# Kernel tuning notes

Hardware: AMD Instinct MI355X
Metric: run time of the kernel (lower is better)

The kernel has to match this reference:

```python
import jax, jax.numpy as jnp
import numpy as np

NEG_SLOPE = 0.2
EPS = 1e-16


def gat_conv(x, src, dst, W, a_src, a_dst, b, num_nodes):
    # Single-head PyG GATConv (heads=1, add_self_loops already applied via src/dst).
    h = x @ W                                   # [N, C]
    alpha_s = h @ a_src                         # [N]
    alpha_d = h @ a_dst                         # [N]
    e = jax.nn.leaky_relu(alpha_s[src] + alpha_d[dst], NEG_SLOPE)  # [E]
    # softmax over incoming edges per destination node
    m = jax.ops.segment_max(e, dst, num_segments=num_nodes)        # [N]
    ex = jnp.exp(e - m[dst])
    denom = jax.ops.segment_sum(ex, dst, num_segments=num_nodes)   # [N]
    alpha = ex / (denom[dst] + EPS)                                 # [E]
    out = jax.ops.segment_sum(h[src] * alpha[:, None], dst, num_segments=num_nodes)
    return out + b


def setup_inputs() -> dict:
    key = jax.random.key(0)
    ks = jax.random.split(key, 10)
    N, E, F_in, H, C = 100000, 1600000, 64, 64, 32
    x = jax.random.normal(ks[0], (N, F_in), dtype=jnp.float32)
    edge_index = jax.random.randint(ks[1], (2, E), 0, N, dtype=jnp.int64)
    s1 = 1.0 / np.sqrt(F_in)
    s2 = 1.0 / np.sqrt(H)
    return {
        "x": x,
        "edge_index": edge_index,
        "W1": jax.random.normal(ks[2], (F_in, H), dtype=jnp.float32) * s1,
        "a1_src": jax.random.normal(ks[3], (H,), dtype=jnp.float32) * s2,
        "a1_dst": jax.random.normal(ks[4], (H,), dtype=jnp.float32) * s2,
        "b1": jnp.zeros((H,), dtype=jnp.float32),
        "W2": jax.random.normal(ks[5], (H, C), dtype=jnp.float32) * s2,
        "a2_src": jax.random.normal(ks[6], (C,), dtype=jnp.float32) / np.sqrt(C),
        "a2_dst": jax.random.normal(ks[7], (C,), dtype=jnp.float32) / np.sqrt(C),
        "b2": jnp.zeros((C,), dtype=jnp.float32),
    }


def reference(x, edge_index, W1, a1_src, a1_dst, b1, W2, a2_src, a2_dst, b2):
    N = x.shape[0]
    loops = jnp.arange(N, dtype=edge_index.dtype)
    src = jnp.concatenate([edge_index[0], loops])  # add self-loops (GATConv default)
    dst = jnp.concatenate([edge_index[1], loops])
    # dropout layers are no-ops in eval mode
    h = jax.nn.relu(gat_conv(x, src, dst, W1, a1_src, a1_dst, b1, N))
    out = gat_conv(h, src, dst, W2, a2_src, a2_dst, b2, N)
    return jax.nn.log_softmax(out, axis=-1)
```

## Files before the change

kernel.cpp:

```cpp
#include <hip/hip_runtime.h>

typedef unsigned int uint;
typedef unsigned short ushort;
typedef short short8 __attribute__((ext_vector_type(8)));
typedef float floatx4 __attribute__((ext_vector_type(4)));

#define LEAKY(e) ((e) > 0.f ? (e) : 0.2f * (e))
#define BCAP 6144
#define EPT 32
#define TILE (256 * EPT)

__device__ __forceinline__ ushort f2bf(float f) {
    uint u = __float_as_uint(f);
    return (ushort)((u + 0x7fffu + ((u >> 16) & 1u)) >> 16);
}
__device__ __forceinline__ float bflo(uint u) { return __uint_as_float(u << 16); }
__device__ __forceinline__ float bfhi(uint u) { return __uint_as_float(u & 0xffff0000u); }

__global__ __launch_bounds__(256) void gemm1_mfma(
    const float* __restrict__ x, const float* __restrict__ W,
    const float* __restrict__ a_src, const float* __restrict__ a_dst,
    ushort* __restrict__ hb, float* __restrict__ as, float* __restrict__ ad, int N)
{
    int tid = threadIdx.x;
    int wave = tid >> 6, lane = tid & 63;
    int q = lane >> 4, c0 = lane & 15;
    int rowbase = blockIdx.x * 64 + wave * 16;
    int arow = rowbase + c0;
    bool aok = arow < N;

    short8 afrag[2];
#pragma unroll
    for (int kb = 0; kb < 2; ++kb) {
        float xa[8];
        if (aok) {
            const float4 u0 = *(const float4*)(x + (size_t)arow * 64 + kb * 32 + q * 8);
            const float4 u1 = *(const float4*)(x + (size_t)arow * 64 + kb * 32 + q * 8 + 4);
            xa[0] = u0.x; xa[1] = u0.y; xa[2] = u0.z; xa[3] = u0.w;
            xa[4] = u1.x; xa[5] = u1.y; xa[6] = u1.z; xa[7] = u1.w;
        } else {
#pragma unroll
            for (int j = 0; j < 8; ++j) xa[j] = 0.f;
        }
#pragma unroll
        for (int j = 0; j < 8; ++j) afrag[kb][j] = (short)f2bf(xa[j]);
    }

    short8 bfrag[4][2];
#pragma unroll
    for (int t = 0; t < 4; ++t)
#pragma unroll
        for (int kb = 0; kb < 2; ++kb)
#pragma unroll
            for (int j = 0; j < 8; ++j)
                bfrag[t][kb][j] = (short)f2bf(W[(size_t)(kb * 32 + q * 8 + j) * 64 + t * 16 + c0]);

    floatx4 acc[4];
#pragma unroll
    for (int t = 0; t < 4; ++t) acc[t] = (floatx4){0.f, 0.f, 0.f, 0.f};
#pragma unroll
    for (int t = 0; t < 4; ++t)
#pragma unroll
        for (int kb = 0; kb < 2; ++kb)
            acc[t] = __builtin_amdgcn_mfma_f32_16x16x32_bf16(afrag[kb], bfrag[t][kb], acc[t], 0, 0, 0);

    float a_s[4], a_d[4];
#pragma unroll
    for (int t = 0; t < 4; ++t) { a_s[t] = a_src[t * 16 + c0]; a_d[t] = a_dst[t * 16 + c0]; }
    float vs[4], vd[4];
#pragma unroll
    for (int r = 0; r < 4; ++r) {
        vs[r] = 0.f; vd[r] = 0.f;
#pragma unroll
        for (int t = 0; t < 4; ++t) { vs[r] += acc[t][r] * a_s[t]; vd[r] += acc[t][r] * a_d[t]; }
    }
#pragma unroll
    for (int o = 1; o < 16; o <<= 1)
#pragma unroll
        for (int r = 0; r < 4; ++r) {
            vs[r] += __shfl_xor(vs[r], o, 16);
            vd[r] += __shfl_xor(vd[r], o, 16);
        }
    int drow = rowbase + q * 4;
    if (c0 == 0) {
#pragma unroll
        for (int r = 0; r < 4; ++r)
            if (drow + r < N) { as[drow + r] = vs[r]; ad[drow + r] = vd[r]; }
    }
#pragma unroll
    for (int r = 0; r < 4; ++r) {
        if (drow + r < N) {
#pragma unroll
            for (int t = 0; t < 4; ++t)
                hb[(size_t)(drow + r) * 64 + t * 16 + c0] = f2bf(acc[t][r]);
        }
    }
}

__global__ __launch_bounds__(256) void gemm2_mfma(
    const float* __restrict__ agg1, const float* __restrict__ b1,
    const float* __restrict__ W,
    const float* __restrict__ a_src, const float* __restrict__ a_dst,
    ushort* __restrict__ hb, float* __restrict__ as, float* __restrict__ ad, int N)
{
    int tid = threadIdx.x;
    int wave = tid >> 6, lane = tid & 63;
    int q = lane >> 4, c0 = lane & 15;
    int rowbase = blockIdx.x * 64 + wave * 16;
    int arow = rowbase + c0;
    bool aok = arow < N;

    short8 afrag[2];
#pragma unroll
    for (int kb = 0; kb < 2; ++kb) {
        float xa[8];
        const float4 b0 = *(const float4*)(b1 + kb * 32 + q * 8);
        const float4 b4 = *(const float4*)(b1 + kb * 32 + q * 8 + 4);
        if (aok) {
            const float4 u0 = *(const float4*)(agg1 + (size_t)arow * 64 + kb * 32 + q * 8);
            const float4 u1 = *(const float4*)(agg1 + (size_t)arow * 64 + kb * 32 + q * 8 + 4);
            xa[0] = u0.x + b0.x; xa[1] = u0.y + b0.y; xa[2] = u0.z + b0.z; xa[3] = u0.w + b0.w;
            xa[4] = u1.x + b4.x; xa[5] = u1.y + b4.y; xa[6] = u1.z + b4.z; xa[7] = u1.w + b4.w;
#pragma unroll
            for (int j = 0; j < 8; ++j) xa[j] = xa[j] > 0.f ? xa[j] : 0.f;
        } else {
#pragma unroll
            for (int j = 0; j < 8; ++j) xa[j] = 0.f;
        }
#pragma unroll
        for (int j = 0; j < 8; ++j) afrag[kb][j] = (short)f2bf(xa[j]);
    }

    short8 bfrag[2][2];
#pragma unroll
    for (int t = 0; t < 2; ++t)
#pragma unroll
        for (int kb = 0; kb < 2; ++kb)
#pragma unroll
            for (int j = 0; j < 8; ++j)
                bfrag[t][kb][j] = (short)f2bf(W[(size_t)(kb * 32 + q * 8 + j) * 32 + t * 16 + c0]);

    floatx4 acc[2];
#pragma unroll
    for (int t = 0; t < 2; ++t) acc[t] = (floatx4){0.f, 0.f, 0.f, 0.f};
#pragma unroll
    for (int t = 0; t < 2; ++t)
#pragma unroll
        for (int kb = 0; kb < 2; ++kb)
            acc[t] = __builtin_amdgcn_mfma_f32_16x16x32_bf16(afrag[kb], bfrag[t][kb], acc[t], 0, 0, 0);

    float a_s[2], a_d[2];
#pragma unroll
    for (int t = 0; t < 2; ++t) { a_s[t] = a_src[t * 16 + c0]; a_d[t] = a_dst[t * 16 + c0]; }
    float vs[4], vd[4];
#pragma unroll
    for (int r = 0; r < 4; ++r) {
        vs[r] = 0.f; vd[r] = 0.f;
#pragma unroll
        for (int t = 0; t < 2; ++t) { vs[r] += acc[t][r] * a_s[t]; vd[r] += acc[t][r] * a_d[t]; }
    }
#pragma unroll
    for (int o = 1; o < 16; o <<= 1)
#pragma unroll
        for (int r = 0; r < 4; ++r) {
            vs[r] += __shfl_xor(vs[r], o, 16);
            vd[r] += __shfl_xor(vd[r], o, 16);
        }
    int drow = rowbase + q * 4;
    if (c0 == 0) {
#pragma unroll
        for (int r = 0; r < 4; ++r)
            if (drow + r < N) { as[drow + r] = vs[r]; ad[drow + r] = vd[r]; }
    }
#pragma unroll
    for (int r = 0; r < 4; ++r) {
        if (drow + r < N) {
#pragma unroll
            for (int t = 0; t < 2; ++t)
                hb[(size_t)(drow + r) * 32 + t * 16 + c0] = f2bf(acc[t][r]);
        }
    }
}

__global__ __launch_bounds__(256) void binK(
    const int* __restrict__ srcA, const int* __restrict__ dstA,
    int* __restrict__ bcur, int* __restrict__ binned, int E, int Etot, int nbuck)
{
    __shared__ int hist[512];
    __shared__ int basep[512];
    int t = threadIdx.x;
    long long start = (long long)blockIdx.x * TILE;

    hist[t] = 0; hist[t + 256] = 0;
    __syncthreads();

    short bs[EPT];
    int vals[EPT];
#pragma unroll
    for (int j = 0; j < EPT; ++j) {
        long long i = start + (long long)j * 256 + t;
        if (i < Etot) {
            int s, d;
            if (i < E) { s = srcA[i]; d = dstA[i]; } else { s = d = (int)(i - E); }
            int b = d >> 8;
            bs[j] = (short)b;
            vals[j] = (s << 8) | (d & 255);
            atomicAdd(&hist[b], 1);
        } else bs[j] = -1;
    }
    __syncthreads();

    for (int b = t; b < nbuck; b += 256) {
        int hc = hist[b];
        basep[b] = hc ? atomicAdd(bcur + b * 16, hc) : 0;
    }
    __syncthreads();
    hist[t] = 0; hist[t + 256] = 0;
    __syncthreads();

#pragma unroll
    for (int j = 0; j < EPT; ++j) {
        int b = bs[j];
        if (b >= 0) {
            int pos = basep[b] + atomicAdd(&hist[b], 1);
            if (pos < BCAP) binned[(size_t)b * BCAP + pos] = vals[j];
        }
    }
}

__global__ __launch_bounds__(256) void bucketK(
    const int* __restrict__ bcur, const int* __restrict__ binned,
    int* __restrict__ off, int* __restrict__ csr, int N, int nbuck)
{
    __shared__ int hist[256];
    __shared__ int sh[256];
    __shared__ int cur[256];
    int b = blockIdx.x;
    int t = threadIdx.x;
    int cnt = min(bcur[b * 16], BCAP);
    const int* bin = binned + (size_t)b * BCAP;

    int partial = 0;
    for (int i = t; i < b; i += 256) partial += min(bcur[i * 16], BCAP);
    sh[t] = partial;
    __syncthreads();
#pragma unroll
    for (int o = 128; o > 0; o >>= 1) {
        if (t < o) sh[t] += sh[t + o];
        __syncthreads();
    }
    int base = sh[0];
    __syncthreads();

    hist[t] = 0;
    __syncthreads();
    for (int i = t; i < cnt; i += 256) atomicAdd(&hist[bin[i] & 255], 1);
    __syncthreads();
    int v = hist[t];
    sh[t] = v;
    __syncthreads();
#pragma unroll
    for (int o = 1; o < 256; o <<= 1) {
        int u = (t >= o) ? sh[t - o] : 0;
        __syncthreads();
        sh[t] += u;
        __syncthreads();
    }
    int excl = sh[t] - v;
    int d = b * 256 + t;
    if (d < N) off[d] = base + excl;
    if (b == nbuck - 1 && t == 0) off[N] = base + cnt;
    cur[t] = base + excl;
    __syncthreads();
    for (int i = t; i < cnt; i += 256) {
        int e = bin[i];
        int p = atomicAdd(&cur[e & 255], 1);
        csr[p] = e >> 8;
    }
}

__global__ __launch_bounds__(256) void node_agg1(
    const int* __restrict__ csr_src, const int* __restrict__ off,
    const float* __restrict__ as, const float* __restrict__ ad,
    const ushort* __restrict__ hb, float* __restrict__ agg, int N)
{
    int tid = threadIdx.x;
    int lid = tid & 7;
    int n = blockIdx.x * 32 + (tid >> 3);
    if (n >= N) return;
    int p0 = off[n], p1 = off[n + 1];
    float adn = ad[n];

    float den = 0.f;
    float acc[8];
#pragma unroll
    for (int k = 0; k < 8; ++k) acc[k] = 0.f;

    int p = p0;
    for (; p + 3 < p1; p += 4) {
        int s0 = csr_src[p], s1 = csr_src[p + 1], s2 = csr_src[p + 2], s3 = csr_src[p + 3];
        float e0 = as[s0], e1 = as[s1], e2 = as[s2], e3 = as[s3];
        const uint4 v0 = *(const uint4*)(hb + (size_t)s0 * 64 + lid * 8);
        const uint4 v1 = *(const uint4*)(hb + (size_t)s1 * 64 + lid * 8);
        const uint4 v2 = *(const uint4*)(hb + (size_t)s2 * 64 + lid * 8);
        const uint4 v3 = *(const uint4*)(hb + (size_t)s3 * 64 + lid * 8);
        float w0 = __expf(LEAKY(e0 + adn));
        float w1 = __expf(LEAKY(e1 + adn));
        float w2 = __expf(LEAKY(e2 + adn));
        float w3 = __expf(LEAKY(e3 + adn));
        den += (w0 + w1) + (w2 + w3);
        acc[0] += w0 * bflo(v0.x); acc[1] += w0 * bfhi(v0.x);
        acc[2] += w0 * bflo(v0.y); acc[3] += w0 * bfhi(v0.y);
        acc[4] += w0 * bflo(v0.z); acc[5] += w0 * bfhi(v0.z);
        acc[6] += w0 * bflo(v0.w); acc[7] += w0 * bfhi(v0.w);
        acc[0] += w1 * bflo(v1.x); acc[1] += w1 * bfhi(v1.x);
        acc[2] += w1 * bflo(v1.y); acc[3] += w1 * bfhi(v1.y);
        acc[4] += w1 * bflo(v1.z); acc[5] += w1 * bfhi(v1.z);
        acc[6] += w1 * bflo(v1.w); acc[7] += w1 * bfhi(v1.w);
        acc[0] += w2 * bflo(v2.x); acc[1] += w2 * bfhi(v2.x);
        acc[2] += w2 * bflo(v2.y); acc[3] += w2 * bfhi(v2.y);
        acc[4] += w2 * bflo(v2.z); acc[5] += w2 * bfhi(v2.z);
        acc[6] += w2 * bflo(v2.w); acc[7] += w2 * bfhi(v2.w);
        acc[0] += w3 * bflo(v3.x); acc[1] += w3 * bfhi(v3.x);
        acc[2] += w3 * bflo(v3.y); acc[3] += w3 * bfhi(v3.y);
        acc[4] += w3 * bflo(v3.z); acc[5] += w3 * bfhi(v3.z);
        acc[6] += w3 * bflo(v3.w); acc[7] += w3 * bfhi(v3.w);
    }
    for (; p < p1; ++p) {
        int s0 = csr_src[p];
        float w0 = __expf(LEAKY(as[s0] + adn));
        const uint4 v0 = *(const uint4*)(hb + (size_t)s0 * 64 + lid * 8);
        den += w0;
        acc[0] += w0 * bflo(v0.x); acc[1] += w0 * bfhi(v0.x);
        acc[2] += w0 * bflo(v0.y); acc[3] += w0 * bfhi(v0.y);
        acc[4] += w0 * bflo(v0.z); acc[5] += w0 * bfhi(v0.z);
        acc[6] += w0 * bflo(v0.w); acc[7] += w0 * bfhi(v0.w);
    }
    float inv = 1.f / den;
    float4 o0 = make_float4(acc[0] * inv, acc[1] * inv, acc[2] * inv, acc[3] * inv);
    float4 o1 = make_float4(acc[4] * inv, acc[5] * inv, acc[6] * inv, acc[7] * inv);
    float* op = agg + (size_t)n * 64 + lid * 8;
    *(float4*)op = o0;
    *(float4*)(op + 4) = o1;
}

__global__ __launch_bounds__(256) void node_agg2(
    const int* __restrict__ csr_src, const int* __restrict__ off,
    const float* __restrict__ as, const float* __restrict__ ad,
    const ushort* __restrict__ hb, const float* __restrict__ b2,
    float* __restrict__ out, int N)
{
    int tid = threadIdx.x;
    int lid = tid & 3;
    int n = blockIdx.x * 64 + (tid >> 2);
    if (n >= N) return;
    int p0 = off[n], p1 = off[n + 1];
    float adn = ad[n];

    float den = 0.f;
    float acc[8];
#pragma unroll
    for (int k = 0; k < 8; ++k) acc[k] = 0.f;

    int p = p0;
    for (; p + 3 < p1; p += 4) {
        int s0 = csr_src[p], s1 = csr_src[p + 1], s2 = csr_src[p + 2], s3 = csr_src[p + 3];
        float e0 = as[s0], e1 = as[s1], e2 = as[s2], e3 = as[s3];
        const uint4 v0 = *(const uint4*)(hb + (size_t)s0 * 32 + lid * 8);
        const uint4 v1 = *(const uint4*)(hb + (size_t)s1 * 32 + lid * 8);
        const uint4 v2 = *(const uint4*)(hb + (size_t)s2 * 32 + lid * 8);
        const uint4 v3 = *(const uint4*)(hb + (size_t)s3 * 32 + lid * 8);
        float w0 = __expf(LEAKY(e0 + adn));
        float w1 = __expf(LEAKY(e1 + adn));
        float w2 = __expf(LEAKY(e2 + adn));
        float w3 = __expf(LEAKY(e3 + adn));
        den += (w0 + w1) + (w2 + w3);
        acc[0] += w0 * bflo(v0.x); acc[1] += w0 * bfhi(v0.x);
        acc[2] += w0 * bflo(v0.y); acc[3] += w0 * bfhi(v0.y);
        acc[4] += w0 * bflo(v0.z); acc[5] += w0 * bfhi(v0.z);
        acc[6] += w0 * bflo(v0.w); acc[7] += w0 * bfhi(v0.w);
        acc[0] += w1 * bflo(v1.x); acc[1] += w1 * bfhi(v1.x);
        acc[2] += w1 * bflo(v1.y); acc[3] += w1 * bfhi(v1.y);
        acc[4] += w1 * bflo(v1.z); acc[5] += w1 * bfhi(v1.z);
        acc[6] += w1 * bflo(v1.w); acc[7] += w1 * bfhi(v1.w);
        acc[0] += w2 * bflo(v2.x); acc[1] += w2 * bfhi(v2.x);
        acc[2] += w2 * bflo(v2.y); acc[3] += w2 * bfhi(v2.y);
        acc[4] += w2 * bflo(v2.z); acc[5] += w2 * bfhi(v2.z);
        acc[6] += w2 * bflo(v2.w); acc[7] += w2 * bfhi(v2.w);
        acc[0] += w3 * bflo(v3.x); acc[1] += w3 * bfhi(v3.x);
        acc[2] += w3 * bflo(v3.y); acc[3] += w3 * bfhi(v3.y);
        acc[4] += w3 * bflo(v3.z); acc[5] += w3 * bfhi(v3.z);
        acc[6] += w3 * bflo(v3.w); acc[7] += w3 * bfhi(v3.w);
    }
    for (; p < p1; ++p) {
        int s0 = csr_src[p];
        float w0 = __expf(LEAKY(as[s0] + adn));
        const uint4 v0 = *(const uint4*)(hb + (size_t)s0 * 32 + lid * 8);
        den += w0;
        acc[0] += w0 * bflo(v0.x); acc[1] += w0 * bfhi(v0.x);
        acc[2] += w0 * bflo(v0.y); acc[3] += w0 * bfhi(v0.y);
        acc[4] += w0 * bflo(v0.z); acc[5] += w0 * bfhi(v0.z);
        acc[6] += w0 * bflo(v0.w); acc[7] += w0 * bfhi(v0.w);
    }
    float inv = 1.f / den;
#pragma unroll
    for (int k = 0; k < 8; ++k) acc[k] = acc[k] * inv + b2[lid * 8 + k];

    float mx = acc[0];
#pragma unroll
    for (int k = 1; k < 8; ++k) mx = fmaxf(mx, acc[k]);
#pragma unroll
    for (int o = 2; o > 0; o >>= 1) mx = fmaxf(mx, __shfl_xor(mx, o, 4));
    float se = 0.f;
#pragma unroll
    for (int k = 0; k < 8; ++k) se += __expf(acc[k] - mx);
#pragma unroll
    for (int o = 2; o > 0; o >>= 1) se += __shfl_xor(se, o, 4);
    float lse = mx + __logf(se);
    float4 o0 = make_float4(acc[0] - lse, acc[1] - lse, acc[2] - lse, acc[3] - lse);
    float4 o1 = make_float4(acc[4] - lse, acc[5] - lse, acc[6] - lse, acc[7] - lse);
    float* op = out + (size_t)n * 32 + lid * 8;
    *(float4*)op = o0;
    *(float4*)(op + 4) = o1;
}

extern "C" void kernel_launch(void* const* d_in, const int* in_sizes, int n_in,
                              void* d_out, int out_size, void* d_ws, size_t ws_size,
                              hipStream_t stream) {
    const float* x   = (const float*)d_in[0];
    const int*   ei  = (const int*)d_in[1];
    const float* W1  = (const float*)d_in[2];
    const float* a1s = (const float*)d_in[3];
    const float* a1d = (const float*)d_in[4];
    const float* b1  = (const float*)d_in[5];
    const float* W2  = (const float*)d_in[6];
    const float* a2s = (const float*)d_in[7];
    const float* a2d = (const float*)d_in[8];
    const float* b2  = (const float*)d_in[9];

    int N = in_sizes[0] / 64;
    int E = in_sizes[1] / 2;
    int Etot = E + N;
    int nbuck = (N + 255) >> 8;
    const int* srcA = ei;
    const int* dstA = ei + E;

    float* ws = (float*)d_ws;
    ushort* hb1 = (ushort*)ws;
    float* agg1 = ws + (size_t)N * 32;
    ushort* hb2 = (ushort*)(agg1 + (size_t)N * 64);
    float* as1  = agg1 + (size_t)N * 64 + (size_t)N * 16;
    float* ad1  = as1 + N;
    float* as2  = ad1 + N;
    float* ad2  = as2 + N;
    int* off    = (int*)(ad2 + N);
    int* bcur   = off + (N + 1);
    int* csr    = bcur + (size_t)nbuck * 16;
    int* binned = csr + Etot;

    hipMemsetAsync(bcur, 0, sizeof(int) * (size_t)nbuck * 16, stream);

    int tb = (int)(((long long)Etot + TILE - 1) / TILE);
    binK<<<tb, 256, 0, stream>>>(srcA, dstA, bcur, binned, E, Etot, nbuck);
    bucketK<<<nbuck, 256, 0, stream>>>(bcur, binned, off, csr, N, nbuck);

    gemm1_mfma<<<(N + 63) / 64, 256, 0, stream>>>(x, W1, a1s, a1d, hb1, as1, ad1, N);
    node_agg1<<<(N + 31) / 32, 256, 0, stream>>>(csr, off, as1, ad1, hb1, agg1, N);

    gemm2_mfma<<<(N + 63) / 64, 256, 0, stream>>>(agg1, b1, W2, a2s, a2d, hb2, as2, ad2, N);
    node_agg2<<<(N + 63) / 64, 256, 0, stream>>>(csr, off, as2, ad2, hb2, b2,
                                                 (float*)d_out, N);
}
```

Measured before the change: 225.1 us.

## Fuse edge binning with first GEMM, cooperative edge gathers, bf16 layer-1 aggregate

```diff
diff --git a/kernel.cpp b/kernel.cpp
--- a/kernel.cpp
+++ b/kernel.cpp
@@ -14,182 +14,20 @@
     uint u = __float_as_uint(f);
     return (ushort)((u + 0x7fffu + ((u >> 16) & 1u)) >> 16);
 }
+__device__ __forceinline__ uint pack2bf(float lo, float hi) {
+    return (uint)f2bf(lo) | ((uint)f2bf(hi) << 16);
+}
 __device__ __forceinline__ float bflo(uint u) { return __uint_as_float(u << 16); }
 __device__ __forceinline__ float bfhi(uint u) { return __uint_as_float(u & 0xffff0000u); }
 
-__global__ __launch_bounds__(256) void gemm1_mfma(
-    const float* __restrict__ x, const float* __restrict__ W,
-    const float* __restrict__ a_src, const float* __restrict__ a_dst,
-    ushort* __restrict__ hb, float* __restrict__ as, float* __restrict__ ad, int N)
-{
-    int tid = threadIdx.x;
-    int wave = tid >> 6, lane = tid & 63;
-    int q = lane >> 4, c0 = lane & 15;
-    int rowbase = blockIdx.x * 64 + wave * 16;
-    int arow = rowbase + c0;
-    bool aok = arow < N;
-
-    short8 afrag[2];
-#pragma unroll
-    for (int kb = 0; kb < 2; ++kb) {
-        float xa[8];
-        if (aok) {
-            const float4 u0 = *(const float4*)(x + (size_t)arow * 64 + kb * 32 + q * 8);
-            const float4 u1 = *(const float4*)(x + (size_t)arow * 64 + kb * 32 + q * 8 + 4);
-            xa[0] = u0.x; xa[1] = u0.y; xa[2] = u0.z; xa[3] = u0.w;
-            xa[4] = u1.x; xa[5] = u1.y; xa[6] = u1.z; xa[7] = u1.w;
-        } else {
-#pragma unroll
-            for (int j = 0; j < 8; ++j) xa[j] = 0.f;
-        }
-#pragma unroll
-        for (int j = 0; j < 8; ++j) afrag[kb][j] = (short)f2bf(xa[j]);
-    }
-
-    short8 bfrag[4][2];
-#pragma unroll
-    for (int t = 0; t < 4; ++t)
-#pragma unroll
-        for (int kb = 0; kb < 2; ++kb)
-#pragma unroll
-            for (int j = 0; j < 8; ++j)
-                bfrag[t][kb][j] = (short)f2bf(W[(size_t)(kb * 32 + q * 8 + j) * 64 + t * 16 + c0]);
-
-    floatx4 acc[4];
-#pragma unroll
-    for (int t = 0; t < 4; ++t) acc[t] = (floatx4){0.f, 0.f, 0.f, 0.f};
-#pragma unroll
-    for (int t = 0; t < 4; ++t)
-#pragma unroll
-        for (int kb = 0; kb < 2; ++kb)
-            acc[t] = __builtin_amdgcn_mfma_f32_16x16x32_bf16(afrag[kb], bfrag[t][kb], acc[t], 0, 0, 0);
-
-    float a_s[4], a_d[4];
-#pragma unroll
-    for (int t = 0; t < 4; ++t) { a_s[t] = a_src[t * 16 + c0]; a_d[t] = a_dst[t * 16 + c0]; }
-    float vs[4], vd[4];
-#pragma unroll
-    for (int r = 0; r < 4; ++r) {
-        vs[r] = 0.f; vd[r] = 0.f;
-#pragma unroll
-        for (int t = 0; t < 4; ++t) { vs[r] += acc[t][r] * a_s[t]; vd[r] += acc[t][r] * a_d[t]; }
-    }
-#pragma unroll
-    for (int o = 1; o < 16; o <<= 1)
-#pragma unroll
-        for (int r = 0; r < 4; ++r) {
-            vs[r] += __shfl_xor(vs[r], o, 16);
-            vd[r] += __shfl_xor(vd[r], o, 16);
-        }
-    int drow = rowbase + q * 4;
-    if (c0 == 0) {
-#pragma unroll
-        for (int r = 0; r < 4; ++r)
-            if (drow + r < N) { as[drow + r] = vs[r]; ad[drow + r] = vd[r]; }
-    }
-#pragma unroll
-    for (int r = 0; r < 4; ++r) {
-        if (drow + r < N) {
-#pragma unroll
-            for (int t = 0; t < 4; ++t)
-                hb[(size_t)(drow + r) * 64 + t * 16 + c0] = f2bf(acc[t][r]);
-        }
-    }
-}
-
-__global__ __launch_bounds__(256) void gemm2_mfma(
-    const float* __restrict__ agg1, const float* __restrict__ b1,
-    const float* __restrict__ W,
-    const float* __restrict__ a_src, const float* __restrict__ a_dst,
-    ushort* __restrict__ hb, float* __restrict__ as, float* __restrict__ ad, int N)
-{
-    int tid = threadIdx.x;
-    int wave = tid >> 6, lane = tid & 63;
-    int q = lane >> 4, c0 = lane & 15;
-    int rowbase = blockIdx.x * 64 + wave * 16;
-    int arow = rowbase + c0;
-    bool aok = arow < N;
-
-    short8 afrag[2];
-#pragma unroll
-    for (int kb = 0; kb < 2; ++kb) {
-        float xa[8];
-        const float4 b0 = *(const float4*)(b1 + kb * 32 + q * 8);
-        const float4 b4 = *(const float4*)(b1 + kb * 32 + q * 8 + 4);
-        if (aok) {
-            const float4 u0 = *(const float4*)(agg1 + (size_t)arow * 64 + kb * 32 + q * 8);
-            const float4 u1 = *(const float4*)(agg1 + (size_t)arow * 64 + kb * 32 + q * 8 + 4);
-            xa[0] = u0.x + b0.x; xa[1] = u0.y + b0.y; xa[2] = u0.z + b0.z; xa[3] = u0.w + b0.w;
-            xa[4] = u1.x + b4.x; xa[5] = u1.y + b4.y; xa[6] = u1.z + b4.z; xa[7] = u1.w + b4.w;
-#pragma unroll
-            for (int j = 0; j < 8; ++j) xa[j] = xa[j] > 0.f ? xa[j] : 0.f;
-        } else {
-#pragma unroll
-            for (int j = 0; j < 8; ++j) xa[j] = 0.f;
-        }
-#pragma unroll
-        for (int j = 0; j < 8; ++j) afrag[kb][j] = (short)f2bf(xa[j]);
-    }
-
-    short8 bfrag[2][2];
-#pragma unroll
-    for (int t = 0; t < 2; ++t)
-#pragma unroll
-        for (int kb = 0; kb < 2; ++kb)
-#pragma unroll
-            for (int j = 0; j < 8; ++j)
-                bfrag[t][kb][j] = (short)f2bf(W[(size_t)(kb * 32 + q * 8 + j) * 32 + t * 16 + c0]);
-
-    floatx4 acc[2];
-#pragma unroll
-    for (int t = 0; t < 2; ++t) acc[t] = (floatx4){0.f, 0.f, 0.f, 0.f};
-#pragma unroll
-    for (int t = 0; t < 2; ++t)
-#pragma unroll
-        for (int kb = 0; kb < 2; ++kb)
-            acc[t] = __builtin_amdgcn_mfma_f32_16x16x32_bf16(afrag[kb], bfrag[t][kb], acc[t], 0, 0, 0);
-
-    float a_s[2], a_d[2];
-#pragma unroll
-    for (int t = 0; t < 2; ++t) { a_s[t] = a_src[t * 16 + c0]; a_d[t] = a_dst[t * 16 + c0]; }
-    float vs[4], vd[4];
-#pragma unroll
-    for (int r = 0; r < 4; ++r) {
-        vs[r] = 0.f; vd[r] = 0.f;
-#pragma unroll
-        for (int t = 0; t < 2; ++t) { vs[r] += acc[t][r] * a_s[t]; vd[r] += acc[t][r] * a_d[t]; }
-    }
-#pragma unroll
-    for (int o = 1; o < 16; o <<= 1)
-#pragma unroll
-        for (int r = 0; r < 4; ++r) {
-            vs[r] += __shfl_xor(vs[r], o, 16);
-            vd[r] += __shfl_xor(vd[r], o, 16);
-        }
-    int drow = rowbase + q * 4;
-    if (c0 == 0) {
-#pragma unroll
-        for (int r = 0; r < 4; ++r)
-            if (drow + r < N) { as[drow + r] = vs[r]; ad[drow + r] = vd[r]; }
-    }
-#pragma unroll
-    for (int r = 0; r < 4; ++r) {
-        if (drow + r < N) {
-#pragma unroll
-            for (int t = 0; t < 2; ++t)
-                hb[(size_t)(drow + r) * 32 + t * 16 + c0] = f2bf(acc[t][r]);
-        }
-    }
-}
-
-__global__ __launch_bounds__(256) void binK(
-    const int* __restrict__ srcA, const int* __restrict__ dstA,
+__device__ __forceinline__ void binK_body(
+    int bid, const int* __restrict__ srcA, const int* __restrict__ dstA,
     int* __restrict__ bcur, int* __restrict__ binned, int E, int Etot, int nbuck)
 {
     __shared__ int hist[512];
     __shared__ int basep[512];
     int t = threadIdx.x;
-    long long start = (long long)blockIdx.x * TILE;
+    long long start = (long long)bid * TILE;
 
     hist[t] = 0; hist[t + 256] = 0;
     __syncthreads();
@@ -228,6 +66,184 @@
     }
 }
 
+__device__ __forceinline__ void gemm1_body(
+    int bid, const float* __restrict__ x, const float* __restrict__ W,
+    const float* __restrict__ a_src, const float* __restrict__ a_dst,
+    ushort* __restrict__ hb, float* __restrict__ as, float* __restrict__ ad, int N)
+{
+    int tid = threadIdx.x;
+    int wave = tid >> 6, lane = tid & 63;
+    int q = lane >> 4, c0 = lane & 15;
+    int rowbase = bid * 64 + wave * 16;
+    int arow = rowbase + c0;
+    bool aok = arow < N;
+
+    short8 afrag[2];
+#pragma unroll
+    for (int kb = 0; kb < 2; ++kb) {
+        float xa[8];
+        if (aok) {
+            const float4 u0 = *(const float4*)(x + (size_t)arow * 64 + kb * 32 + q * 8);
+            const float4 u1 = *(const float4*)(x + (size_t)arow * 64 + kb * 32 + q * 8 + 4);
+            xa[0] = u0.x; xa[1] = u0.y; xa[2] = u0.z; xa[3] = u0.w;
+            xa[4] = u1.x; xa[5] = u1.y; xa[6] = u1.z; xa[7] = u1.w;
+        } else {
+#pragma unroll
+            for (int j = 0; j < 8; ++j) xa[j] = 0.f;
+        }
+#pragma unroll
+        for (int j = 0; j < 8; ++j) afrag[kb][j] = (short)f2bf(xa[j]);
+    }
+
+    short8 bfrag[4][2];
+#pragma unroll
+    for (int t = 0; t < 4; ++t)
+#pragma unroll
+        for (int kb = 0; kb < 2; ++kb)
+#pragma unroll
+            for (int j = 0; j < 8; ++j)
+                bfrag[t][kb][j] = (short)f2bf(W[(size_t)(kb * 32 + q * 8 + j) * 64 + t * 16 + c0]);
+
+    floatx4 acc[4];
+#pragma unroll
+    for (int t = 0; t < 4; ++t) acc[t] = (floatx4){0.f, 0.f, 0.f, 0.f};
+#pragma unroll
+    for (int t = 0; t < 4; ++t)
+#pragma unroll
+        for (int kb = 0; kb < 2; ++kb)
+            acc[t] = __builtin_amdgcn_mfma_f32_16x16x32_bf16(afrag[kb], bfrag[t][kb], acc[t], 0, 0, 0);
+
+    float a_s[4], a_d[4];
+#pragma unroll
+    for (int t = 0; t < 4; ++t) { a_s[t] = a_src[t * 16 + c0]; a_d[t] = a_dst[t * 16 + c0]; }
+    float vs[4], vd[4];
+#pragma unroll
+    for (int r = 0; r < 4; ++r) {
+        vs[r] = 0.f; vd[r] = 0.f;
+#pragma unroll
+        for (int t = 0; t < 4; ++t) { vs[r] += acc[t][r] * a_s[t]; vd[r] += acc[t][r] * a_d[t]; }
+    }
+#pragma unroll
+    for (int o = 1; o < 16; o <<= 1)
+#pragma unroll
+        for (int r = 0; r < 4; ++r) {
+            vs[r] += __shfl_xor(vs[r], o, 16);
+            vd[r] += __shfl_xor(vd[r], o, 16);
+        }
+    int drow = rowbase + q * 4;
+    if (c0 == 0) {
+#pragma unroll
+        for (int r = 0; r < 4; ++r)
+            if (drow + r < N) { as[drow + r] = vs[r]; ad[drow + r] = vd[r]; }
+    }
+#pragma unroll
+    for (int r = 0; r < 4; ++r) {
+        if (drow + r < N) {
+#pragma unroll
+            for (int t = 0; t < 4; ++t)
+                hb[(size_t)(drow + r) * 64 + t * 16 + c0] = f2bf(acc[t][r]);
+        }
+    }
+}
+
+__global__ __launch_bounds__(256) void fusedK(
+    const int* __restrict__ srcA, const int* __restrict__ dstA,
+    int* __restrict__ bcur, int* __restrict__ binned, int E, int Etot, int nbuck, int tb,
+    const float* __restrict__ x, const float* __restrict__ W,
+    const float* __restrict__ a_src, const float* __restrict__ a_dst,
+    ushort* __restrict__ hb, float* __restrict__ as, float* __restrict__ ad, int N)
+{
+    int b = (int)blockIdx.x;
+    if (b < tb) binK_body(b, srcA, dstA, bcur, binned, E, Etot, nbuck);
+    else gemm1_body(b - tb, x, W, a_src, a_dst, hb, as, ad, N);
+}
+
+__global__ __launch_bounds__(256) void gemm2_mfma(
+    const ushort* __restrict__ aggb, const float* __restrict__ b1,
+    const float* __restrict__ W,
+    const float* __restrict__ a_src, const float* __restrict__ a_dst,
+    ushort* __restrict__ hb, float* __restrict__ as, float* __restrict__ ad, int N)
+{
+    int tid = threadIdx.x;
+    int wave = tid >> 6, lane = tid & 63;
+    int q = lane >> 4, c0 = lane & 15;
+    int rowbase = blockIdx.x * 64 + wave * 16;
+    int arow = rowbase + c0;
+    bool aok = arow < N;
+
+    short8 afrag[2];
+#pragma unroll
+    for (int kb = 0; kb < 2; ++kb) {
+        float xa[8];
+        const float4 b0 = *(const float4*)(b1 + kb * 32 + q * 8);
+        const float4 b4 = *(const float4*)(b1 + kb * 32 + q * 8 + 4);
+        if (aok) {
+            const uint4 u = *(const uint4*)(aggb + (size_t)arow * 64 + kb * 32 + q * 8);
+            xa[0] = bflo(u.x) + b0.x; xa[1] = bfhi(u.x) + b0.y;
+            xa[2] = bflo(u.y) + b0.z; xa[3] = bfhi(u.y) + b0.w;
+            xa[4] = bflo(u.z) + b4.x; xa[5] = bfhi(u.z) + b4.y;
+            xa[6] = bflo(u.w) + b4.z; xa[7] = bfhi(u.w) + b4.w;
+#pragma unroll
+            for (int j = 0; j < 8; ++j) xa[j] = xa[j] > 0.f ? xa[j] : 0.f;
+        } else {
+#pragma unroll
+            for (int j = 0; j < 8; ++j) xa[j] = 0.f;
+        }
+#pragma unroll
+        for (int j = 0; j < 8; ++j) afrag[kb][j] = (short)f2bf(xa[j]);
+    }
+
+    short8 bfrag[2][2];
+#pragma unroll
+    for (int t = 0; t < 2; ++t)
+#pragma unroll
+        for (int kb = 0; kb < 2; ++kb)
+#pragma unroll
+            for (int j = 0; j < 8; ++j)
+                bfrag[t][kb][j] = (short)f2bf(W[(size_t)(kb * 32 + q * 8 + j) * 32 + t * 16 + c0]);
+
+    floatx4 acc[2];
+#pragma unroll
+    for (int t = 0; t < 2; ++t) acc[t] = (floatx4){0.f, 0.f, 0.f, 0.f};
+#pragma unroll
+    for (int t = 0; t < 2; ++t)
+#pragma unroll
+        for (int kb = 0; kb < 2; ++kb)
+            acc[t] = __builtin_amdgcn_mfma_f32_16x16x32_bf16(afrag[kb], bfrag[t][kb], acc[t], 0, 0, 0);
+
+    float a_s[2], a_d[2];
+#pragma unroll
+    for (int t = 0; t < 2; ++t) { a_s[t] = a_src[t * 16 + c0]; a_d[t] = a_dst[t * 16 + c0]; }
+    float vs[4], vd[4];
+#pragma unroll
+    for (int r = 0; r < 4; ++r) {
+        vs[r] = 0.f; vd[r] = 0.f;
+#pragma unroll
+        for (int t = 0; t < 2; ++t) { vs[r] += acc[t][r] * a_s[t]; vd[r] += acc[t][r] * a_d[t]; }
+    }
+#pragma unroll
+    for (int o = 1; o < 16; o <<= 1)
+#pragma unroll
+        for (int r = 0; r < 4; ++r) {
+            vs[r] += __shfl_xor(vs[r], o, 16);
+            vd[r] += __shfl_xor(vd[r], o, 16);
+        }
+    int drow = rowbase + q * 4;
+    if (c0 == 0) {
+#pragma unroll
+        for (int r = 0; r < 4; ++r)
+            if (drow + r < N) { as[drow + r] = vs[r]; ad[drow + r] = vd[r]; }
+    }
+#pragma unroll
+    for (int r = 0; r < 4; ++r) {
+        if (drow + r < N) {
+#pragma unroll
+            for (int t = 0; t < 2; ++t)
+                hb[(size_t)(drow + r) * 32 + t * 16 + c0] = f2bf(acc[t][r]);
+        }
+    }
+}
+
 __global__ __launch_bounds__(256) void bucketK(
     const int* __restrict__ bcur, const int* __restrict__ binned,
     int* __restrict__ off, int* __restrict__ csr, int N, int nbuck)
@@ -282,7 +298,7 @@
 __global__ __launch_bounds__(256) void node_agg1(
     const int* __restrict__ csr_src, const int* __restrict__ off,
     const float* __restrict__ as, const float* __restrict__ ad,
-    const ushort* __restrict__ hb, float* __restrict__ agg, int N)
+    const ushort* __restrict__ hb, ushort* __restrict__ aggb, int N)
 {
     int tid = threadIdx.x;
     int lid = tid & 7;
@@ -296,52 +312,54 @@
 #pragma unroll
     for (int k = 0; k < 8; ++k) acc[k] = 0.f;
 
-    int p = p0;
-    for (; p + 3 < p1; p += 4) {
-        int s0 = csr_src[p], s1 = csr_src[p + 1], s2 = csr_src[p + 2], s3 = csr_src[p + 3];
-        float e0 = as[s0], e1 = as[s1], e2 = as[s2], e3 = as[s3];
-        const uint4 v0 = *(const uint4*)(hb + (size_t)s0 * 64 + lid * 8);
-        const uint4 v1 = *(const uint4*)(hb + (size_t)s1 * 64 + lid * 8);
-        const uint4 v2 = *(const uint4*)(hb + (size_t)s2 * 64 + lid * 8);
-        const uint4 v3 = *(const uint4*)(hb + (size_t)s3 * 64 + lid * 8);
-        float w0 = __expf(LEAKY(e0 + adn));
-        float w1 = __expf(LEAKY(e1 + adn));
-        float w2 = __expf(LEAKY(e2 + adn));
-        float w3 = __expf(LEAKY(e3 + adn));
-        den += (w0 + w1) + (w2 + w3);
-        acc[0] += w0 * bflo(v0.x); acc[1] += w0 * bfhi(v0.x);
-        acc[2] += w0 * bflo(v0.y); acc[3] += w0 * bfhi(v0.y);
-        acc[4] += w0 * bflo(v0.z); acc[5] += w0 * bfhi(v0.z);
-        acc[6] += w0 * bflo(v0.w); acc[7] += w0 * bfhi(v0.w);
-        acc[0] += w1 * bflo(v1.x); acc[1] += w1 * bfhi(v1.x);
-        acc[2] += w1 * bflo(v1.y); acc[3] += w1 * bfhi(v1.y);
-        acc[4] += w1 * bflo(v1.z); acc[5] += w1 * bfhi(v1.z);
-        acc[6] += w1 * bflo(v1.w); acc[7] += w1 * bfhi(v1.w);
-        acc[0] += w2 * bflo(v2.x); acc[1] += w2 * bfhi(v2.x);
-        acc[2] += w2 * bflo(v2.y); acc[3] += w2 * bfhi(v2.y);
-        acc[4] += w2 * bflo(v2.z); acc[5] += w2 * bfhi(v2.z);
-        acc[6] += w2 * bflo(v2.w); acc[7] += w2 * bfhi(v2.w);
-        acc[0] += w3 * bflo(v3.x); acc[1] += w3 * bfhi(v3.x);
-        acc[2] += w3 * bflo(v3.y); acc[3] += w3 * bfhi(v3.y);
-        acc[4] += w3 * bflo(v3.z); acc[5] += w3 * bfhi(v3.z);
-        acc[6] += w3 * bflo(v3.w); acc[7] += w3 * bfhi(v3.w);
-    }
-    for (; p < p1; ++p) {
-        int s0 = csr_src[p];
-        float w0 = __expf(LEAKY(as[s0] + adn));
-        const uint4 v0 = *(const uint4*)(hb + (size_t)s0 * 64 + lid * 8);
-        den += w0;
-        acc[0] += w0 * bflo(v0.x); acc[1] += w0 * bfhi(v0.x);
-        acc[2] += w0 * bflo(v0.y); acc[3] += w0 * bfhi(v0.y);
-        acc[4] += w0 * bflo(v0.z); acc[5] += w0 * bfhi(v0.z);
-        acc[6] += w0 * bflo(v0.w); acc[7] += w0 * bfhi(v0.w);
-    }
+    int base = p0;
+    for (; base + 8 <= p1; base += 8) {
+        int s_l = csr_src[base + lid];
+        float a_l = as[s_l];
+        uint4 v[8];
+#pragma unroll
+        for (int j = 0; j < 8; ++j) {
+            int s_j = __shfl(s_l, j, 8);
+            v[j] = *(const uint4*)(hb + (size_t)s_j * 64 + lid * 8);
+        }
+        float w_l = __expf(LEAKY(a_l + adn));
+        den += w_l;
+#pragma unroll
+        for (int j = 0; j < 8; ++j) {
+            float w = __shfl(w_l, j, 8);
+            acc[0] += w * bflo(v[j].x); acc[1] += w * bfhi(v[j].x);
+            acc[2] += w * bflo(v[j].y); acc[3] += w * bfhi(v[j].y);
+            acc[4] += w * bflo(v[j].z); acc[5] += w * bfhi(v[j].z);
+            acc[6] += w * bflo(v[j].w); acc[7] += w * bfhi(v[j].w);
+        }
+    }
+    int r = p1 - base;
+    if (r) {
+        int s_l = 0; float w_l = 0.f;
+        if (lid < r) { s_l = csr_src[base + lid]; w_l = __expf(LEAKY(as[s_l] + adn)); }
+        den += w_l;
+#pragma unroll
+        for (int j = 0; j < 8; ++j) {
+            if (j < r) {
+                int s_j = __shfl(s_l, j, 8);
+                float w = __shfl(w_l, j, 8);
+                const uint4 v = *(const uint4*)(hb + (size_t)s_j * 64 + lid * 8);
+                acc[0] += w * bflo(v.x); acc[1] += w * bfhi(v.x);
+                acc[2] += w * bflo(v.y); acc[3] += w * bfhi(v.y);
+                acc[4] += w * bflo(v.z); acc[5] += w * bfhi(v.z);
+                acc[6] += w * bflo(v.w); acc[7] += w * bfhi(v.w);
+            }
+        }
+    }
+#pragma unroll
+    for (int o = 4; o > 0; o >>= 1) den += __shfl_xor(den, o, 8);
     float inv = 1.f / den;
-    float4 o0 = make_float4(acc[0] * inv, acc[1] * inv, acc[2] * inv, acc[3] * inv);
-    float4 o1 = make_float4(acc[4] * inv, acc[5] * inv, acc[6] * inv, acc[7] * inv);
-    float* op = agg + (size_t)n * 64 + lid * 8;
-    *(float4*)op = o0;
-    *(float4*)(op + 4) = o1;
+    uint4 o4;
+    o4.x = pack2bf(acc[0] * inv, acc[1] * inv);
+    o4.y = pack2bf(acc[2] * inv, acc[3] * inv);
+    o4.z = pack2bf(acc[4] * inv, acc[5] * inv);
+    o4.w = pack2bf(acc[6] * inv, acc[7] * inv);
+    *(uint4*)(aggb + (size_t)n * 64 + lid * 8) = o4;
 }
 
 __global__ __launch_bounds__(256) void node_agg2(
@@ -362,46 +380,47 @@
 #pragma unroll
     for (int k = 0; k < 8; ++k) acc[k] = 0.f;
 
-    int p = p0;
-    for (; p + 3 < p1; p += 4) {
-        int s0 = csr_src[p], s1 = csr_src[p + 1], s2 = csr_src[p + 2], s3 = csr_src[p + 3];
-        float e0 = as[s0], e1 = as[s1], e2 = as[s2], e3 = as[s3];
-        const uint4 v0 = *(const uint4*)(hb + (size_t)s0 * 32 + lid * 8);
-        const uint4 v1 = *(const uint4*)(hb + (size_t)s1 * 32 + lid * 8);
-        const uint4 v2 = *(const uint4*)(hb + (size_t)s2 * 32 + lid * 8);
-        const uint4 v3 = *(const uint4*)(hb + (size_t)s3 * 32 + lid * 8);
-        float w0 = __expf(LEAKY(e0 + adn));
-        float w1 = __expf(LEAKY(e1 + adn));
-        float w2 = __expf(LEAKY(e2 + adn));
-        float w3 = __expf(LEAKY(e3 + adn));
-        den += (w0 + w1) + (w2 + w3);
-        acc[0] += w0 * bflo(v0.x); acc[1] += w0 * bfhi(v0.x);
-        acc[2] += w0 * bflo(v0.y); acc[3] += w0 * bfhi(v0.y);
-        acc[4] += w0 * bflo(v0.z); acc[5] += w0 * bfhi(v0.z);
-        acc[6] += w0 * bflo(v0.w); acc[7] += w0 * bfhi(v0.w);
-        acc[0] += w1 * bflo(v1.x); acc[1] += w1 * bfhi(v1.x);
-        acc[2] += w1 * bflo(v1.y); acc[3] += w1 * bfhi(v1.y);
-        acc[4] += w1 * bflo(v1.z); acc[5] += w1 * bfhi(v1.z);
-        acc[6] += w1 * bflo(v1.w); acc[7] += w1 * bfhi(v1.w);
-        acc[0] += w2 * bflo(v2.x); acc[1] += w2 * bfhi(v2.x);
-        acc[2] += w2 * bflo(v2.y); acc[3] += w2 * bfhi(v2.y);
-        acc[4] += w2 * bflo(v2.z); acc[5] += w2 * bfhi(v2.z);
-        acc[6] += w2 * bflo(v2.w); acc[7] += w2 * bfhi(v2.w);
-        acc[0] += w3 * bflo(v3.x); acc[1] += w3 * bfhi(v3.x);
-        acc[2] += w3 * bflo(v3.y); acc[3] += w3 * bfhi(v3.y);
-        acc[4] += w3 * bflo(v3.z); acc[5] += w3 * bfhi(v3.z);
-        acc[6] += w3 * bflo(v3.w); acc[7] += w3 * bfhi(v3.w);
-    }
-    for (; p < p1; ++p) {
-        int s0 = csr_src[p];
-        float w0 = __expf(LEAKY(as[s0] + adn));
-        const uint4 v0 = *(const uint4*)(hb + (size_t)s0 * 32 + lid * 8);
-        den += w0;
-        acc[0] += w0 * bflo(v0.x); acc[1] += w0 * bfhi(v0.x);
-        acc[2] += w0 * bflo(v0.y); acc[3] += w0 * bfhi(v0.y);
-        acc[4] += w0 * bflo(v0.z); acc[5] += w0 * bfhi(v0.z);
-        acc[6] += w0 * bflo(v0.w); acc[7] += w0 * bfhi(v0.w);
-    }
+    int base = p0;
+    for (; base + 4 <= p1; base += 4) {
+        int s_l = csr_src[base + lid];
+        float a_l = as[s_l];
+        uint4 v[4];
+#pragma unroll
+        for (int j = 0; j < 4; ++j) {
+            int s_j = __shfl(s_l, j, 4);
+            v[j] = *(const uint4*)(hb + (size_t)s_j * 32 + lid * 8);
+        }
+        float w_l = __expf(LEAKY(a_l + adn));
+        den += w_l;
+#pragma unroll
+        for (int j = 0; j < 4; ++j) {
+            float w = __shfl(w_l, j, 4);
+            acc[0] += w * bflo(v[j].x); acc[1] += w * bfhi(v[j].x);
+            acc[2] += w * bflo(v[j].y); acc[3] += w * bfhi(v[j].y);
+            acc[4] += w * bflo(v[j].z); acc[5] += w * bfhi(v[j].z);
+            acc[6] += w * bflo(v[j].w); acc[7] += w * bfhi(v[j].w);
+        }
+    }
+    int r = p1 - base;
+    if (r) {
+        int s_l = 0; float w_l = 0.f;
+        if (lid < r) { s_l = csr_src[base + lid]; w_l = __expf(LEAKY(as[s_l] + adn)); }
+        den += w_l;
+#pragma unroll
+        for (int j = 0; j < 4; ++j) {
+            if (j < r) {
+                int s_j = __shfl(s_l, j, 4);
+                float w = __shfl(w_l, j, 4);
+                const uint4 v = *(const uint4*)(hb + (size_t)s_j * 32 + lid * 8);
+                acc[0] += w * bflo(v.x); acc[1] += w * bfhi(v.x);
+                acc[2] += w * bflo(v.y); acc[3] += w * bfhi(v.y);
+                acc[4] += w * bflo(v.z); acc[5] += w * bfhi(v.z);
+                acc[6] += w * bflo(v.w); acc[7] += w * bfhi(v.w);
+            }
+        }
+    }
+#pragma unroll
+    for (int o = 2; o > 0; o >>= 1) den += __shfl_xor(den, o, 4);
     float inv = 1.f / den;
 #pragma unroll
     for (int k = 0; k < 8; ++k) acc[k] = acc[k] * inv + b2[lid * 8 + k];
@@ -446,28 +465,28 @@
     const int* dstA = ei + E;
 
     float* ws = (float*)d_ws;
-    ushort* hb1 = (ushort*)ws;
-    float* agg1 = ws + (size_t)N * 32;
-    ushort* hb2 = (ushort*)(agg1 + (size_t)N * 64);
-    float* as1  = agg1 + (size_t)N * 64 + (size_t)N * 16;
-    float* ad1  = as1 + N;
-    float* as2  = ad1 + N;
-    float* ad2  = as2 + N;
-    int* off    = (int*)(ad2 + N);
-    int* bcur   = off + (N + 1);
-    int* csr    = bcur + (size_t)nbuck * 16;
-    int* binned = csr + Etot;
+    ushort* hb1  = (ushort*)ws;
+    ushort* aggb = hb1 + (size_t)N * 64;
+    ushort* hb2  = aggb + (size_t)N * 64;
+    float* as1   = ws + (size_t)N * (32 + 32 + 16);
+    float* ad1   = as1 + N;
+    float* as2   = ad1 + N;
+    float* ad2   = as2 + N;
+    int* off     = (int*)(ad2 + N);
+    int* bcur    = off + (N + 1);
+    int* csr     = bcur + (size_t)nbuck * 16;
+    int* binned  = csr + Etot;
 
     hipMemsetAsync(bcur, 0, sizeof(int) * (size_t)nbuck * 16, stream);
 
     int tb = (int)(((long long)Etot + TILE - 1) / TILE);
-    binK<<<tb, 256, 0, stream>>>(srcA, dstA, bcur, binned, E, Etot, nbuck);
+    int g1 = (N + 63) / 64;
+
+    fusedK<<<tb + g1, 256, 0, stream>>>(srcA, dstA, bcur, binned, E, Etot, nbuck, tb,
+                                        x, W1, a1s, a1d, hb1, as1, ad1, N);
     bucketK<<<nbuck, 256, 0, stream>>>(bcur, binned, off, csr, N, nbuck);
-
-    gemm1_mfma<<<(N + 63) / 64, 256, 0, stream>>>(x, W1, a1s, a1d, hb1, as1, ad1, N);
-    node_agg1<<<(N + 31) / 32, 256, 0, stream>>>(csr, off, as1, ad1, hb1, agg1, N);
-
-    gemm2_mfma<<<(N + 63) / 64, 256, 0, stream>>>(agg1, b1, W2, a2s, a2d, hb2, as2, ad2, N);
+    node_agg1<<<(N + 31) / 32, 256, 0, stream>>>(csr, off, as1, ad1, hb1, aggb, N);
+    gemm2_mfma<<<g1, 256, 0, stream>>>(aggb, b1, W2, a2s, a2d, hb2, as2, ad2, N);
     node_agg2<<<(N + 63) / 64, 256, 0, stream>>>(csr, off, as2, ad2, hb2, b2,
                                                  (float*)d_out, N);
 }
```

Result: faster. 213.2 us (-5.3%).
